# Kernel tuning notes

Measured on AMD Instinct MI355X. Metric: run time of the kernel, lower is better.

## Reference

```python
import jax, jax.numpy as jnp
import numpy as np
from jax import lax

I, H, B, T = 2048, 96, 64, 512

def _rnn_layer(x_in, w_ih, b_ih, w_hh, b_hh):
    """One tanh-RNN layer. x_in: [B, T, D]. Returns [B, T, H]."""
    # Hoist the big input GEMM out of the scan (one batched matmul).
    xproj = jnp.einsum('btd,hd->bth', x_in, w_ih) + b_ih  # [B, T, H]
    def step(h, xt):  # h: [B, H], xt: [B, H]
        h = jnp.tanh(xt + h @ w_hh.T + b_hh)
        return h, h
    h0 = jnp.zeros((x_in.shape[0], w_hh.shape[0]), dtype=x_in.dtype)
    _, ys = lax.scan(step, h0, jnp.swapaxes(xproj, 0, 1))  # [T, B, H]
    return jnp.swapaxes(ys, 0, 1)

def setup_inputs() -> dict:
    key = jax.random.key(0)
    ks = jax.random.split(key, 12)
    s = 0.05  # keep pre-activations in tanh's linear-ish range
    x = jax.random.normal(ks[0], (B, T, I), dtype=jnp.float32)
    return {
        'x': x,
        'w_ih0': jax.random.normal(ks[1], (H, I), jnp.float32) * s,
        'w_hh0': jax.random.normal(ks[2], (H, H), jnp.float32) * s,
        'b_ih0': jnp.zeros((H,), jnp.float32),
        'b_hh0': jnp.zeros((H,), jnp.float32),
        'w_ih1': jax.random.normal(ks[3], (H, H), jnp.float32) * s,
        'w_hh1': jax.random.normal(ks[4], (H, H), jnp.float32) * s,
        'b_ih1': jnp.zeros((H,), jnp.float32),
        'b_hh1': jnp.zeros((H,), jnp.float32),
        'w_ih2': jax.random.normal(ks[5], (H, H), jnp.float32) * s,
        'w_hh2': jax.random.normal(ks[6], (H, H), jnp.float32) * s,
        'b_ih2': jnp.zeros((H,), jnp.float32),
        'b_hh2': jnp.zeros((H,), jnp.float32),
        'fc_w': jax.random.normal(ks[7], (1, H), jnp.float32) * s,
        'fc_b': jnp.zeros((1,), jnp.float32),
    }

def reference(x, w_ih0, w_hh0, b_ih0, b_hh0,
              w_ih1, w_hh1, b_ih1, b_hh1,
              w_ih2, w_hh2, b_ih2, b_hh2,
              fc_w, fc_b):
    # 3-layer tanh RNN (eval mode: inter-layer dropout p=0.1 and head dropout
    # p=0.2 are identity), then last-timestep linear head.
    h1 = _rnn_layer(x,  w_ih0, b_ih0, w_hh0, b_hh0)  # [B, T, H]
    h2 = _rnn_layer(h1, w_ih1, b_ih1, w_hh1, b_hh1)
    h3 = _rnn_layer(h2, w_ih2, b_ih2, w_hh2, b_hh2)
    last = h3[:, -1, :]                               # [B, H]
    return last @ fc_w.T + fc_b                       # [B, 1]
```

## Files before the change

kernel.cpp:

```cpp
#include <hip/hip_runtime.h>
#include <hip/hip_bf16.h>

#define T_STEPS 512
#define B_SZ 64
#define H_SZ 96
#define I_SZ 2048

#define BM 64
#define BN 96
#define BK 32

__global__ __launch_bounds__(256) void xproj_gemm(
    const float* __restrict__ x,
    const float* __restrict__ w,
    const float* __restrict__ bias,
    float* __restrict__ out)
{
    __shared__ float xs[BK][BM + 4];
    __shared__ float ws[BK][BN + 4];

    const int tid = threadIdx.x;
    const int m0 = blockIdx.x * BM;
    const int tm = tid & 15;
    const int tn = tid >> 4;

    float acc[4][6];
#pragma unroll
    for (int r = 0; r < 4; ++r)
#pragma unroll
        for (int c = 0; c < 6; ++c) acc[r][c] = 0.f;

    for (int k0 = 0; k0 < I_SZ; k0 += BK) {
#pragma unroll
        for (int it = 0; it < 2; ++it) {
            int L = tid + it * 256;
            int m = L >> 3;
            int k4 = (L & 7) * 4;
            float4 v = *(const float4*)&x[(size_t)(m0 + m) * I_SZ + k0 + k4];
            xs[k4 + 0][m] = v.x; xs[k4 + 1][m] = v.y;
            xs[k4 + 2][m] = v.z; xs[k4 + 3][m] = v.w;
        }
#pragma unroll
        for (int it = 0; it < 3; ++it) {
            int L = tid + it * 256;
            int j = L >> 3;
            int k4 = (L & 7) * 4;
            float4 v = *(const float4*)&w[(size_t)j * I_SZ + k0 + k4];
            ws[k4 + 0][j] = v.x; ws[k4 + 1][j] = v.y;
            ws[k4 + 2][j] = v.z; ws[k4 + 3][j] = v.w;
        }
        __syncthreads();

#pragma unroll
        for (int k = 0; k < BK; ++k) {
            float a[4], b[6];
#pragma unroll
            for (int r = 0; r < 4; ++r) a[r] = xs[k][tm * 4 + r];
#pragma unroll
            for (int c = 0; c < 6; ++c) b[c] = ws[k][tn * 6 + c];
#pragma unroll
            for (int r = 0; r < 4; ++r)
#pragma unroll
                for (int c = 0; c < 6; ++c) acc[r][c] += a[r] * b[c];
        }
        __syncthreads();
    }

#pragma unroll
    for (int r = 0; r < 4; ++r) {
        int m = m0 + tm * 4 + r;
#pragma unroll
        for (int c = 0; c < 6; ++c) {
            int j = tn * 6 + c;
            out[(size_t)m * H_SZ + j] = acc[r][c] + bias[j];
        }
    }
}


__device__ __forceinline__ float fast_tanh(float x) {
    float cx = fminf(fmaxf(x, -15.f), 15.f);
    float e = __expf(2.f * cx);
    return 1.f - 2.f / (e + 1.f);
}

__global__ __launch_bounds__(512) void rnn3_fused(
    const float* __restrict__ xproj0,
    const float* __restrict__ w_hh0, const float* __restrict__ b_hh0,
    const float* __restrict__ w_ih1, const float* __restrict__ b_ih1,
    const float* __restrict__ w_hh1, const float* __restrict__ b_hh1,
    const float* __restrict__ w_ih2, const float* __restrict__ b_ih2,
    const float* __restrict__ w_hh2, const float* __restrict__ b_hh2,
    const float* __restrict__ fc_w, const float* __restrict__ fc_b,
    float* __restrict__ out)
{
    __shared__ __align__(16) float h0[H_SZ];
    __shared__ __align__(16) float h1[H_SZ];
    __shared__ __align__(16) float h2[H_SZ];
    __shared__ float p1b[H_SZ];
    __shared__ float p2b[H_SZ];
    __shared__ float red[H_SZ];

    const int t = threadIdx.x;
    const int b = blockIdx.x;
    const int g = t / H_SZ;
    const int j = t - g * H_SZ;
    const bool active = (t < 5 * H_SZ);

    float wreg[H_SZ];
    if (active) {
        const float* wp;
        switch (g) {
            case 0: wp = w_hh0; break;
            case 1: wp = w_ih1; break;
            case 2: wp = w_hh1; break;
            case 3: wp = w_ih2; break;
            default: wp = w_hh2; break;
        }
        const float* wrow = wp + j * H_SZ;
#pragma unroll
        for (int k = 0; k < H_SZ; k += 4) {
            float4 v = *(const float4*)&wrow[k];
            wreg[k] = v.x; wreg[k + 1] = v.y; wreg[k + 2] = v.z; wreg[k + 3] = v.w;
        }
    }

    float cbias = 0.f;
    if (t < 96)                  cbias = b_hh0[t];
    else if (t < 192)            cbias = b_ih1[t - 96] + b_hh1[t - 96];
    else if (t >= 288 && t < 384) cbias = b_ih2[t - 288] + b_hh2[t - 288];

    if (t < H_SZ) { h0[t] = 0.f; h1[t] = 0.f; h2[t] = 0.f; }
    __syncthreads();

    const float* xp_base = xproj0 + (size_t)b * T_STEPS * H_SZ;
    float xp_cur = (t < 96) ? xp_base[t] : 0.f;

    for (int i = 0; i < T_STEPS + 2; ++i) {
        float xp_next = 0.f;
        if (t < 96) {
            int ii = (i + 1 < T_STEPS) ? (i + 1) : (T_STEPS - 1);
            xp_next = xp_base[(size_t)ii * H_SZ + t];
        }

        float part = 0.f;
        if (active) {
            const float* hs = (g <= 1) ? h0 : (g <= 3) ? h1 : h2;
            float a0 = 0.f, a1 = 0.f, a2 = 0.f, a3 = 0.f;
#pragma unroll
            for (int k = 0; k < H_SZ; k += 4) {
                float4 hv = *(const float4*)&hs[k];
                a0 += wreg[k]     * hv.x;
                a1 += wreg[k + 1] * hv.y;
                a2 += wreg[k + 2] * hv.z;
                a3 += wreg[k + 3] * hv.w;
            }
            part = (a0 + a1) + (a2 + a3);
            if (g == 2) p1b[j] = part;
            else if (g == 4) p2b[j] = part;
        }
        __syncthreads();

        if (t < 96) {
            if (i < T_STEPS) h0[j] = fast_tanh(xp_cur + part + cbias);
        } else if (t < 192) {
            if (i >= 1 && i <= T_STEPS) h1[j] = fast_tanh(part + p1b[j] + cbias);
        } else if (t >= 288 && t < 384) {
            if (i >= 2) h2[j] = fast_tanh(part + p2b[j] + cbias);
        }
        __syncthreads();

        xp_cur = xp_next;
    }

    if (t < H_SZ) red[t] = h2[t] * fc_w[t];
    __syncthreads();
    if (t == 0) {
        float s = 0.f;
#pragma unroll
        for (int k = 0; k < H_SZ; ++k) s += red[k];
        out[b] = s + fc_b[0];
    }
}

extern "C" void kernel_launch(void* const* d_in, const int* in_sizes, int n_in,
                              void* d_out, int out_size, void* d_ws, size_t ws_size,
                              hipStream_t stream) {
    const float* x     = (const float*)d_in[0];
    const float* w_ih0 = (const float*)d_in[1];
    const float* w_hh0 = (const float*)d_in[2];
    const float* b_ih0 = (const float*)d_in[3];
    const float* b_hh0 = (const float*)d_in[4];
    const float* w_ih1 = (const float*)d_in[5];
    const float* w_hh1 = (const float*)d_in[6];
    const float* b_ih1 = (const float*)d_in[7];
    const float* b_hh1 = (const float*)d_in[8];
    const float* w_ih2 = (const float*)d_in[9];
    const float* w_hh2 = (const float*)d_in[10];
    const float* b_ih2 = (const float*)d_in[11];
    const float* b_hh2 = (const float*)d_in[12];
    const float* fc_w  = (const float*)d_in[13];
    const float* fc_b  = (const float*)d_in[14];

    float* xproj = (float*)d_ws;

    const int M = B_SZ * T_STEPS;
    xproj_gemm<<<M / BM, 256, 0, stream>>>(x, w_ih0, b_ih0, xproj);
    rnn3_fused<<<B_SZ, 512, 0, stream>>>(xproj,
                                         w_hh0, b_hh0,
                                         w_ih1, b_ih1, w_hh1, b_hh1,
                                         w_ih2, b_ih2, w_hh2, b_hh2,
                                         fc_w, fc_b, (float*)d_out);
}
```

Baseline: 1.018 ms.

## Double-buffer GEMM with direct global-to-LDS loads and restructure RNN recurrence mapping

The input-projection GEMM now stages tiles straight from global memory into swizzled, double-buffered LDS. This overlaps the next tile's load with compute and drops the transpose writes, and outputs are stored as float2. The fused RNN kernel is remapped so each thread group of 4 lanes owns 4 output rows over a quarter of K and reduces with shuffles. It uses ping-pong hidden-state buffers so each timestep needs one barrier instead of two, and preloads xproj chunks into LDS. This adds register and LDS pressure, about 98KB of LDS for the xproj chunk, which limits occupancy.

```diff
diff --git a/kernel.cpp b/kernel.cpp
--- a/kernel.cpp
+++ b/kernel.cpp
@@ -9,6 +9,33 @@
 #define BM 64
 #define BN 96
 #define BK 32
+
+typedef const __attribute__((address_space(1))) void g_void;
+typedef __attribute__((address_space(3))) void l_void;
+
+__device__ __forceinline__ void stage_tile(const float* __restrict__ x,
+                                           const float* __restrict__ w,
+                                           float* xsf, float* wsf,
+                                           int buf, int m0, int k0, int tid) {
+#pragma unroll
+    for (int it = 0; it < 2; ++it) {
+        int L = tid + it * 256;
+        int m = L >> 3;
+        int c = (L & 7) ^ ((L >> 5) & 7);
+        const float* g = &x[(size_t)(m0 + m) * I_SZ + k0 + c * 4];
+        __builtin_amdgcn_global_load_lds((g_void*)g,
+            (l_void*)(xsf + buf * (BM * BK) + L * 4), 16, 0, 0);
+    }
+#pragma unroll
+    for (int it = 0; it < 3; ++it) {
+        int L = tid + it * 256;
+        int j = L >> 3;
+        int c = (L & 7) ^ ((L >> 5) & 7);
+        const float* g = &w[(size_t)j * I_SZ + k0 + c * 4];
+        __builtin_amdgcn_global_load_lds((g_void*)g,
+            (l_void*)(wsf + buf * (BN * BK) + L * 4), 16, 0, 0);
+    }
+}
 
 __global__ __launch_bounds__(256) void xproj_gemm(
     const float* __restrict__ x,
@@ -16,67 +43,80 @@
     const float* __restrict__ bias,
     float* __restrict__ out)
 {
-    __shared__ float xs[BK][BM + 4];
-    __shared__ float ws[BK][BN + 4];
+    __shared__ __align__(16) float xsf[2 * BM * BK];
+    __shared__ __align__(16) float wsf[2 * BN * BK];
 
     const int tid = threadIdx.x;
     const int m0 = blockIdx.x * BM;
     const int tm = tid & 15;
     const int tn = tid >> 4;
 
+    float bb[6];
+#pragma unroll
+    for (int c = 0; c < 6; ++c) bb[c] = bias[tn * 6 + c];
+
+    int aoff[4], boff[6], sb[6];
+    const int sa = tm & 7;
+#pragma unroll
+    for (int r = 0; r < 4; ++r) aoff[r] = (tm * 4 + r) * 8;
+#pragma unroll
+    for (int c = 0; c < 6; ++c) {
+        int j = tn * 6 + c;
+        boff[c] = j * 8;
+        sb[c] = (j >> 2) & 7;
+    }
+
     float acc[4][6];
 #pragma unroll
     for (int r = 0; r < 4; ++r)
 #pragma unroll
         for (int c = 0; c < 6; ++c) acc[r][c] = 0.f;
 
-    for (int k0 = 0; k0 < I_SZ; k0 += BK) {
-#pragma unroll
-        for (int it = 0; it < 2; ++it) {
-            int L = tid + it * 256;
-            int m = L >> 3;
-            int k4 = (L & 7) * 4;
-            float4 v = *(const float4*)&x[(size_t)(m0 + m) * I_SZ + k0 + k4];
-            xs[k4 + 0][m] = v.x; xs[k4 + 1][m] = v.y;
-            xs[k4 + 2][m] = v.z; xs[k4 + 3][m] = v.w;
-        }
-#pragma unroll
-        for (int it = 0; it < 3; ++it) {
-            int L = tid + it * 256;
-            int j = L >> 3;
-            int k4 = (L & 7) * 4;
-            float4 v = *(const float4*)&w[(size_t)j * I_SZ + k0 + k4];
-            ws[k4 + 0][j] = v.x; ws[k4 + 1][j] = v.y;
-            ws[k4 + 2][j] = v.z; ws[k4 + 3][j] = v.w;
+    stage_tile(x, w, xsf, wsf, 0, m0, 0, tid);
+    __syncthreads();
+
+    for (int tile = 0; tile < I_SZ / BK; ++tile) {
+        const int buf = tile & 1;
+        if (tile < I_SZ / BK - 1)
+            stage_tile(x, w, xsf, wsf, buf ^ 1, m0, (tile + 1) * BK, tid);
+
+        const float4* xsb = (const float4*)(xsf + buf * (BM * BK));
+        const float4* wsb = (const float4*)(wsf + buf * (BN * BK));
+#pragma unroll
+        for (int cc = 0; cc < 8; ++cc) {
+            float av[4][4], bv[6][4];
+#pragma unroll
+            for (int r = 0; r < 4; ++r)
+                *(float4*)av[r] = xsb[aoff[r] + (cc ^ sa)];
+#pragma unroll
+            for (int c = 0; c < 6; ++c)
+                *(float4*)bv[c] = wsb[boff[c] + (cc ^ sb[c])];
+#pragma unroll
+            for (int kk = 0; kk < 4; ++kk)
+#pragma unroll
+                for (int r = 0; r < 4; ++r)
+#pragma unroll
+                    for (int c = 0; c < 6; ++c)
+                        acc[r][c] = fmaf(av[r][kk], bv[c][kk], acc[r][c]);
         }
         __syncthreads();
-
-#pragma unroll
-        for (int k = 0; k < BK; ++k) {
-            float a[4], b[6];
-#pragma unroll
-            for (int r = 0; r < 4; ++r) a[r] = xs[k][tm * 4 + r];
-#pragma unroll
-            for (int c = 0; c < 6; ++c) b[c] = ws[k][tn * 6 + c];
-#pragma unroll
-            for (int r = 0; r < 4; ++r)
-#pragma unroll
-                for (int c = 0; c < 6; ++c) acc[r][c] += a[r] * b[c];
-        }
-        __syncthreads();
     }
 
 #pragma unroll
     for (int r = 0; r < 4; ++r) {
-        int m = m0 + tm * 4 + r;
-#pragma unroll
-        for (int c = 0; c < 6; ++c) {
-            int j = tn * 6 + c;
-            out[(size_t)m * H_SZ + j] = acc[r][c] + bias[j];
-        }
-    }
-}
-
+        float* op = &out[(size_t)(m0 + tm * 4 + r) * H_SZ + tn * 6];
+        *(float2*)(op + 0) = make_float2(acc[r][0] + bb[0], acc[r][1] + bb[1]);
+        *(float2*)(op + 2) = make_float2(acc[r][2] + bb[2], acc[r][3] + bb[3]);
+        *(float2*)(op + 4) = make_float2(acc[r][4] + bb[4], acc[r][5] + bb[5]);
+    }
+}
+
+
+#define WQ_LIST(F) \
+    F(0,0) F(0,1) F(0,2) F(0,3) F(0,4) F(0,5) \
+    F(1,0) F(1,1) F(1,2) F(1,3) F(1,4) F(1,5) \
+    F(2,0) F(2,1) F(2,2) F(2,3) F(2,4) F(2,5) \
+    F(3,0) F(3,1) F(3,2) F(3,3) F(3,4) F(3,5)
 
 __device__ __forceinline__ float fast_tanh(float x) {
     float cx = fminf(fmaxf(x, -15.f), 15.f);
@@ -84,7 +124,9 @@
     return 1.f - 2.f / (e + 1.f);
 }
 
-__global__ __launch_bounds__(512) void rnn3_fused(
+#define CHUNK 256
+
+__global__ __launch_bounds__(512, 2) void rnn3_fused(
     const float* __restrict__ xproj0,
     const float* __restrict__ w_hh0, const float* __restrict__ b_hh0,
     const float* __restrict__ w_ih1, const float* __restrict__ b_ih1,
@@ -94,92 +136,98 @@
     const float* __restrict__ fc_w, const float* __restrict__ fc_b,
     float* __restrict__ out)
 {
-    __shared__ __align__(16) float h0[H_SZ];
-    __shared__ __align__(16) float h1[H_SZ];
-    __shared__ __align__(16) float h2[H_SZ];
-    __shared__ float p1b[H_SZ];
-    __shared__ float p2b[H_SZ];
+    __shared__ __align__(16) float xp_ch[CHUNK * H_SZ];
+    __shared__ __align__(16) float hls[2 * 3 * H_SZ];
     __shared__ float red[H_SZ];
 
     const int t = threadIdx.x;
     const int b = blockIdx.x;
-    const int g = t / H_SZ;
-    const int j = t - g * H_SZ;
-    const bool active = (t < 5 * H_SZ);
-
-    float wreg[H_SZ];
-    if (active) {
-        const float* wp;
-        switch (g) {
-            case 0: wp = w_hh0; break;
-            case 1: wp = w_ih1; break;
-            case 2: wp = w_hh1; break;
-            case 3: wp = w_ih2; break;
-            default: wp = w_hh2; break;
+    const int wv = t >> 6;
+    const int l = t & 63;
+
+    int half, q, sub, j0, in_sel, out_sel, layer;
+    const float* mat;
+    if (wv < 6) {
+        half = l >> 5; int lq = l & 31; q = lq >> 2; sub = lq & 3;
+        if (wv < 3) { layer = 1; j0 = wv * 32 + q * 4;
+                      mat = half ? w_hh1 : w_ih1; in_sel = half ? 1 : 0; out_sel = 1; }
+        else        { layer = 2; j0 = (wv - 3) * 32 + q * 4;
+                      mat = half ? w_hh2 : w_ih2; in_sel = half ? 2 : 1; out_sel = 2; }
+    } else {
+        half = 0; q = l >> 2; sub = l & 3; layer = 0;
+        j0 = (wv - 6) * 64 + q * 4;
+        mat = w_hh0; in_sel = 0; out_sel = 0;
+    }
+    const bool jvalid = (j0 < H_SZ);
+    const int j0c = jvalid ? j0 : H_SZ - 4;
+    const int jme = j0c + sub;
+    const float* wrb = mat + j0c * H_SZ + sub * 24;
+
+#define DECLW(r, c) float4 W##r##_##c = *(const float4*)(wrb + (r) * H_SZ + (c) * 4);
+    WQ_LIST(DECLW)
+
+    float cb;
+    if (layer == 0)      cb = b_hh0[jme];
+    else if (layer == 1) cb = b_ih1[jme] + b_hh1[jme];
+    else                 cb = b_ih2[jme] + b_hh2[jme];
+
+    for (int k = t; k < 2 * 3 * H_SZ; k += 512) hls[k] = 0.f;
+    __syncthreads();
+
+    const float* xp_base = xproj0 + (size_t)b * T_STEPS * H_SZ;
+
+    for (int i = 0; i < T_STEPS + 2; ++i) {
+        if ((i & (CHUNK - 1)) == 0 && i < T_STEPS) {
+            const float4* src = (const float4*)(xp_base + (size_t)i * H_SZ);
+            float4* dst = (float4*)xp_ch;
+#pragma unroll
+            for (int qq = 0; qq < 12; ++qq) dst[t + qq * 512] = src[t + qq * 512];
+            __syncthreads();
         }
-        const float* wrow = wp + j * H_SZ;
-#pragma unroll
-        for (int k = 0; k < H_SZ; k += 4) {
-            float4 v = *(const float4*)&wrow[k];
-            wreg[k] = v.x; wreg[k + 1] = v.y; wreg[k + 2] = v.z; wreg[k + 3] = v.w;
-        }
-    }
-
-    float cbias = 0.f;
-    if (t < 96)                  cbias = b_hh0[t];
-    else if (t < 192)            cbias = b_ih1[t - 96] + b_hh1[t - 96];
-    else if (t >= 288 && t < 384) cbias = b_ih2[t - 288] + b_hh2[t - 288];
-
-    if (t < H_SZ) { h0[t] = 0.f; h1[t] = 0.f; h2[t] = 0.f; }
-    __syncthreads();
-
-    const float* xp_base = xproj0 + (size_t)b * T_STEPS * H_SZ;
-    float xp_cur = (t < 96) ? xp_base[t] : 0.f;
-
-    for (int i = 0; i < T_STEPS + 2; ++i) {
-        float xp_next = 0.f;
-        if (t < 96) {
-            int ii = (i + 1 < T_STEPS) ? (i + 1) : (T_STEPS - 1);
-            xp_next = xp_base[(size_t)ii * H_SZ + t];
-        }
-
-        float part = 0.f;
-        if (active) {
-            const float* hs = (g <= 1) ? h0 : (g <= 3) ? h1 : h2;
-            float a0 = 0.f, a1 = 0.f, a2 = 0.f, a3 = 0.f;
-#pragma unroll
-            for (int k = 0; k < H_SZ; k += 4) {
-                float4 hv = *(const float4*)&hs[k];
-                a0 += wreg[k]     * hv.x;
-                a1 += wreg[k + 1] * hv.y;
-                a2 += wreg[k + 2] * hv.z;
-                a3 += wreg[k + 3] * hv.w;
-            }
-            part = (a0 + a1) + (a2 + a3);
-            if (g == 2) p1b[j] = part;
-            else if (g == 4) p2b[j] = part;
+        const int buf = i & 1;
+
+        const float4* hp = (const float4*)&hls[buf * (3 * H_SZ) + in_sel * H_SZ + sub * 24];
+        float4 hv0 = hp[0], hv1 = hp[1], hv2 = hp[2], hv3 = hp[3], hv4 = hp[4], hv5 = hp[5];
+
+        float xpv = 0.f;
+        if (layer == 0) xpv = xp_ch[(i & (CHUNK - 1)) * H_SZ + jme];
+
+        float a0 = 0.f, a1 = 0.f, a2 = 0.f, a3 = 0.f;
+#define DOTQ(r, c) { a##r = fmaf(W##r##_##c.x, hv##c.x, a##r); \
+                     a##r = fmaf(W##r##_##c.y, hv##c.y, a##r); \
+                     a##r = fmaf(W##r##_##c.z, hv##c.z, a##r); \
+                     a##r = fmaf(W##r##_##c.w, hv##c.w, a##r); }
+        WQ_LIST(DOTQ)
+
+        float m0 = (sub & 1) ? a0 : a1;
+        float m1 = (sub & 1) ? a2 : a3;
+        float x0 = __shfl_xor(m0, 1, 64);
+        float x1 = __shfl_xor(m1, 1, 64);
+        float u0 = ((sub & 1) ? a1 : a0) + x0;
+        float u1 = ((sub & 1) ? a3 : a2) + x1;
+        float m2 = (sub & 2) ? u0 : u1;
+        float x2 = __shfl_xor(m2, 2, 64);
+        float fin = ((sub & 2) ? u1 : u0) + x2;
+
+        float fin2 = fin + __shfl_xor(fin, 32, 64);
+
+        float* hn = &hls[(buf ^ 1) * (3 * H_SZ) + out_sel * H_SZ];
+        if (layer == 0) {
+            if (jvalid && i < T_STEPS) hn[jme] = fast_tanh(fin + xpv + cb);
+        } else if (half == 0) {
+            bool ok = (layer == 1) ? (i >= 1 && i <= T_STEPS) : (i >= 2);
+            if (ok) hn[jme] = fast_tanh(fin2 + cb);
         }
         __syncthreads();
-
-        if (t < 96) {
-            if (i < T_STEPS) h0[j] = fast_tanh(xp_cur + part + cbias);
-        } else if (t < 192) {
-            if (i >= 1 && i <= T_STEPS) h1[j] = fast_tanh(part + p1b[j] + cbias);
-        } else if (t >= 288 && t < 384) {
-            if (i >= 2) h2[j] = fast_tanh(part + p2b[j] + cbias);
-        }
-        __syncthreads();
-
-        xp_cur = xp_next;
-    }
-
-    if (t < H_SZ) red[t] = h2[t] * fc_w[t];
+    }
+
+    if (t < H_SZ) red[t] = hls[2 * H_SZ + t] * fc_w[t];
     __syncthreads();
     if (t == 0) {
-        float s = 0.f;
-#pragma unroll
-        for (int k = 0; k < H_SZ; ++k) s += red[k];
-        out[b] = s + fc_b[0];
+        float sm = 0.f;
+#pragma unroll
+        for (int k = 0; k < H_SZ; ++k) sm += red[k];
+        out[b] = sm + fc_b[0];
     }
 }
 
```

Result: faster. 838.4 us (-17.7%).
